# Kernel optimization log

Measured on AMD Instinct MI355X. Metric: run time of the kernel, lower is better.

## Reference

```python
import jax, jax.numpy as jnp
import numpy as np

ROPE_BASE = 10000.0


def _rope_tables(T, d, dtype):
    # inv_freq over even indices, emb = concat(freqs, freqs) -> [T, d]
    inv_freq = 1.0 / (ROPE_BASE ** (jnp.arange(0, d, 2, dtype=jnp.float32) / d))
    t = jnp.arange(T, dtype=jnp.float32)
    freqs = jnp.einsum('i,j->ij', t, inv_freq)          # [T, d/2]
    emb = jnp.concatenate([freqs, freqs], axis=-1)      # [T, d]
    return jnp.cos(emb).astype(dtype), jnp.sin(emb).astype(dtype)


def _rotate_half(x):
    d = x.shape[-1] // 2
    return jnp.concatenate([-x[..., d:], x[..., :d]], axis=-1)


def _apply_rope(x, cos, sin):
    # x: [B, T, H, Dh]; cos/sin: [T, Dh] broadcast over batch and heads
    c = cos[None, :, None, :]
    s = sin[None, :, None, :]
    return x * c + _rotate_half(x) * s


def setup_inputs() -> dict:
    key = jax.random.key(0)
    k1, k2, k3 = jax.random.split(key, 3)
    B, T, C = 2, 2048, 1024
    x = jax.random.normal(k1, (B, T, C), dtype=jnp.float32)
    # weights stored as [in, out] (transposed nn.Linear), scaled like torch init
    W_qkv = jax.random.normal(k2, (C, 3 * C), dtype=jnp.float32) * (C ** -0.5)
    W_proj = jax.random.normal(k3, (C, C), dtype=jnp.float32) * (C ** -0.5)
    return {'x': x, 'W_qkv': W_qkv, 'W_proj': W_proj}


def reference(x, W_qkv, W_proj):
    B, T, C = x.shape
    H = 16
    Dh = C // H
    qkv = x @ W_qkv                                   # [B, T, 3C]
    q, k, v = jnp.split(qkv, 3, axis=-1)
    q = q.reshape(B, T, H, Dh)
    k = k.reshape(B, T, H, Dh)
    v = v.reshape(B, T, H, Dh)
    cos, sin = _rope_tables(T, Dh, x.dtype)
    q = _apply_rope(q, cos, sin)
    k = _apply_rope(k, cos, sin)
    scale = 1.0 / jnp.sqrt(jnp.asarray(Dh, dtype=x.dtype))
    # causal SDPA: scores [B, H, T, T]
    scores = jnp.einsum('bqhd,bkhd->bhqk', q, k) * scale
    causal = jnp.tril(jnp.ones((T, T), dtype=bool))
    scores = jnp.where(causal[None, None], scores, jnp.asarray(-jnp.inf, dtype=scores.dtype))
    attn = jax.nn.softmax(scores, axis=-1)
    y = jnp.einsum('bhqk,bkhd->bqhd', attn, v).reshape(B, T, C)
    return y @ W_proj
```

## Files before the change

### kernel.cpp

```cpp
#include <hip/hip_runtime.h>
#include <cstdint>
#include <cstddef>

typedef __bf16 bf16;
typedef __bf16 bf16x2 __attribute__((ext_vector_type(2)));
typedef __bf16 bf16x4 __attribute__((ext_vector_type(4)));
typedef __bf16 bf16x8 __attribute__((ext_vector_type(8)));
typedef float  f32x4  __attribute__((ext_vector_type(4)));
typedef float  f32x16 __attribute__((ext_vector_type(16)));
typedef int    i32x4  __attribute__((ext_vector_type(4)));

__device__ __forceinline__ float fexp2(float x) {
  float r;
  asm("v_exp_f32 %0, %1" : "=v"(r) : "v"(x));
  return r;
}
__device__ __forceinline__ float m3(float a, float b, float c) {
  return fmaxf(fmaxf(a, b), c);
}

#define G2L(src, dst)                                                          \
  __builtin_amdgcn_global_load_lds(                                            \
      (const __attribute__((address_space(1))) unsigned int*)(src),            \
      (__attribute__((address_space(3))) unsigned int*)(dst), 16, 0, 0)

__global__ void k_f32_to_bf16(const float* __restrict__ in, bf16* __restrict__ out, int n) {
  int i = (blockIdx.x * blockDim.x + threadIdx.x) * 8;
  if (i >= n) return;
  float4 a = *(const float4*)(in + i);
  float4 b = *(const float4*)(in + i + 4);
  bf16x8 o;
  o[0] = (bf16)a.x; o[1] = (bf16)a.y; o[2] = (bf16)a.z; o[3] = (bf16)a.w;
  o[4] = (bf16)b.x; o[5] = (bf16)b.y; o[6] = (bf16)b.z; o[7] = (bf16)b.w;
  *(bf16x8*)(out + i) = o;
}

__global__ void k_transpose_f32_bf16(const float* __restrict__ in, bf16* __restrict__ out,
                                     int R, int C) {
  __shared__ float tile[32][33];
  int c0 = blockIdx.x * 32, r0 = blockIdx.y * 32;
  int tx = threadIdx.x & 31, ty = threadIdx.x >> 5;
#pragma unroll
  for (int i = 0; i < 32; i += 8)
    tile[ty + i][tx] = in[(size_t)(r0 + ty + i) * C + c0 + tx];
  __syncthreads();
#pragma unroll
  for (int i = 0; i < 32; i += 8)
    out[(size_t)(c0 + ty + i) * R + r0 + tx] = (bf16)tile[tx][ty + i];
}

__global__ void k_rope_tables(float* __restrict__ cosT, float* __restrict__ sinT, int total) {
  int i = blockIdx.x * blockDim.x + threadIdx.x;
  if (i >= total) return;
  int t = i >> 5, j = i & 31;
  float inv = powf(10000.0f, -(float)j * (1.0f / 32.0f));
  float f = (float)t * inv;
  cosT[i] = cosf(f);
  sinT[i] = sinf(f);
}

__global__ __launch_bounds__(256) void k_rope_v(const bf16* __restrict__ qkv,
                                                const float* __restrict__ cosT,
                                                const float* __restrict__ sinT,
                                                bf16* __restrict__ qr,
                                                bf16* __restrict__ kr,
                                                bf16* __restrict__ vt) {
  __shared__ bf16 tile[64][66];
  int bh = blockIdx.y;
  int t0 = blockIdx.x * 64;
  int b = bh >> 4, h = bh & 15;
  int tt = threadIdx.x >> 2, g = threadIdx.x & 3;
  int c4 = g * 16;
  const bf16* row = qkv + (size_t)(b * 2048 + t0 + tt) * 3072 + h * 64;
  bf16x8 v0 = *(const bf16x8*)(row + 2048 + c4);
  bf16x8 v1 = *(const bf16x8*)(row + 2048 + c4 + 8);
#pragma unroll
  for (int j = 0; j < 8; j++) { tile[tt][c4 + j] = v0[j]; tile[tt][c4 + 8 + j] = v1[j]; }
  int tglob = t0 + tt;
  size_t ob = ((size_t)bh * 2048 + tglob) * 64;
  const float QS = 0.125f * 1.44269504f;
  bf16x8 qlo = *(const bf16x8*)(row + g * 8);
  bf16x8 qhi = *(const bf16x8*)(row + 32 + g * 8);
  bf16x8 klo = *(const bf16x8*)(row + 1024 + g * 8);
  bf16x8 khi = *(const bf16x8*)(row + 1024 + 32 + g * 8);
  bf16x8 qo0, qo1, ko0, ko1;
#pragma unroll
  for (int j = 0; j < 8; j++) {
    float c = cosT[tglob * 32 + g * 8 + j], s = sinT[tglob * 32 + g * 8 + j];
    float ql = (float)qlo[j], qh = (float)qhi[j];
    float kl = (float)klo[j], kh = (float)khi[j];
    qo0[j] = (bf16)((ql * c - qh * s) * QS);
    qo1[j] = (bf16)((qh * c + ql * s) * QS);
    ko0[j] = (bf16)(kl * c - kh * s);
    ko1[j] = (bf16)(kh * c + kl * s);
  }
  *(bf16x8*)&qr[ob + g * 8]      = qo0;
  *(bf16x8*)&qr[ob + 32 + g * 8] = qo1;
  *(bf16x8*)&kr[ob + g * 8]      = ko0;
  *(bf16x8*)&kr[ob + 32 + g * 8] = ko1;
  __syncthreads();
  int d = threadIdx.x >> 2, tc0 = (threadIdx.x & 3) * 16;
  bf16x8 o0, o1;
#pragma unroll
  for (int j = 0; j < 8; j++) { o0[j] = tile[tc0 + j][d]; o1[j] = tile[tc0 + 8 + j][d]; }
  bf16* dst = vt + ((size_t)bh * 64 + d) * 2048 + t0 + tc0;
  *(bf16x8*)dst = o0;
  *(bf16x8*)(dst + 8) = o1;
}

template <int OUTF32>
__global__ __launch_bounds__(256) void k_gemm_bt(const bf16* __restrict__ A,
                                                 const bf16* __restrict__ Bt,
                                                 float* __restrict__ Cf, bf16* __restrict__ Cb,
                                                 int M, int N, int K) {
  __shared__ __align__(16) bf16 sA[128 * 64];
  __shared__ __align__(16) bf16 sB[128 * 64];
  int nwg = gridDim.x * gridDim.y;
  int idl = blockIdx.y * gridDim.x + blockIdx.x;
  int cpx = nwg >> 3;
  int swz = (idl & 7) * cpx + (idl >> 3);
  int bx = swz % gridDim.x, by = swz / gridDim.x;
  int m0 = by * 128, n0 = bx * 128;
  int t = threadIdx.x, lane = t & 63, w = t >> 6;
  int wr = w >> 1, wc = w & 1;
  int lr = lane & 15, q2 = lane >> 4;
  int srow8 = lane >> 3, pc8 = lane & 7;
  f32x4 acc[4][4] = {};
  for (int k0 = 0; k0 < K; k0 += 64) {
#pragma unroll
    for (int is = 0; is < 4; is++) {
      int r = w * 32 + is * 8 + srow8;
      int lc = pc8 ^ (r & 7);
      G2L(A + (size_t)(m0 + r) * K + k0 + lc * 8, &sA[(w * 32 + is * 8) * 64]);
    }
#pragma unroll
    for (int is = 0; is < 4; is++) {
      int r = w * 32 + is * 8 + srow8;
      int lc = pc8 ^ (r & 7);
      G2L(Bt + (size_t)(n0 + r) * K + k0 + lc * 8, &sB[(w * 32 + is * 8) * 64]);
    }
    __syncthreads();
#pragma unroll
    for (int ch = 0; ch < 2; ch++) {
      bf16x8 af[4], bfr[4];
#pragma unroll
      for (int i = 0; i < 4; i++) {
        int r = wr * 64 + i * 16 + lr;
        af[i] = *(const bf16x8*)&sA[r * 64 + (((ch * 4 + q2) ^ (r & 7)) * 8)];
      }
#pragma unroll
      for (int i = 0; i < 4; i++) {
        int r = wc * 64 + i * 16 + lr;
        bfr[i] = *(const bf16x8*)&sB[r * 64 + (((ch * 4 + q2) ^ (r & 7)) * 8)];
      }
#pragma unroll
      for (int mi = 0; mi < 4; mi++)
#pragma unroll
        for (int ni = 0; ni < 4; ni++)
          acc[mi][ni] = __builtin_amdgcn_mfma_f32_16x16x32_bf16(af[mi], bfr[ni], acc[mi][ni], 0, 0, 0);
    }
    __syncthreads();
  }
  int row_base = m0 + wr * 64, col_base = n0 + wc * 64;
#pragma unroll
  for (int mi = 0; mi < 4; mi++)
#pragma unroll
    for (int ni = 0; ni < 4; ni++) {
      int col = col_base + ni * 16 + lr;
#pragma unroll
      for (int r = 0; r < 4; r++) {
        int row = row_base + mi * 16 + q2 * 4 + r;
        float v = acc[mi][ni][r];
        if (OUTF32) Cf[(size_t)row * N + col] = v;
        else        Cb[(size_t)row * N + col] = (bf16)v;
      }
    }
}

__global__ __launch_bounds__(128) void k_flash_part(const bf16* __restrict__ qr,
                                                    const bf16* __restrict__ kr,
                                                    const bf16* __restrict__ vt,
                                                    bf16* __restrict__ Opart,
                                                    float* __restrict__ ml) {
  const int T = 2048;
  int id = blockIdx.x;
  int slot = id >> 5;
  int bh = id & 31;
  int qt = 31, c = 0;
  {
    int s = slot;
#pragma unroll 1
    for (int q = 31; q >= 0; --q) {
      int n = q / 6 + 1;
      if (s < n) { qt = q; c = s; break; }
      s -= n;
    }
  }
  int kt0 = c * 6;
  int kt1 = qt + 1 < kt0 + 6 ? qt + 1 : kt0 + 6;

  __shared__ __align__(16) bf16 sK[64 * 64];
  __shared__ __align__(16) bf16 sV[64 * 64];
  int t = threadIdx.x, lane = t & 63, w = t >> 6;
  int q31 = lane & 31, hi = lane >> 5;
  int srow8 = lane >> 3, pc8 = lane & 7;

  const bf16* Kbh = kr + (size_t)bh * T * 64;
  const bf16* Vbh = vt + (size_t)bh * 64 * T;

  int qwb = qt * 64 + w * 32;
  int qg = qwb + q31;
  const bf16* qrow = qr + ((size_t)bh * T + qg) * 64 + hi * 8;
  bf16x8 qf[4];
#pragma unroll
  for (int ks = 0; ks < 4; ks++) qf[ks] = *(const bf16x8*)(qrow + ks * 16);
  f32x16 o0 = {}, o1 = {};
  float m = -1e30f, l = 0.f;

  auto stage = [&](int kt) {
#pragma unroll
    for (int is = 0; is < 4; is++) {
      int r = w * 32 + is * 8 + srow8;
      int lc = pc8 ^ (r & 7);
      G2L(Kbh + (size_t)(kt * 64 + r) * 64 + lc * 8, &sK[(w * 32 + is * 8) * 64]);
    }
#pragma unroll
    for (int is = 0; is < 4; is++) {
      int d = w * 32 + is * 8 + srow8;
      int lc = pc8 ^ (d & 7);
      G2L(Vbh + (size_t)d * T + kt * 64 + lc * 8, &sV[(w * 32 + is * 8) * 64]);
    }
  };

  stage(kt0);
  for (int kt = kt0; kt < kt1; kt++) {
    asm volatile("s_waitcnt vmcnt(0)" ::: "memory");
    __builtin_amdgcn_s_barrier();
    asm volatile("" ::: "memory");
    __builtin_amdgcn_sched_barrier(0);
    f32x16 s[2];
    __builtin_amdgcn_s_setprio(1);
#pragma unroll
    for (int kb = 0; kb < 2; kb++) {
      f32x16 a = {};
      int krow = kb * 32 + q31;
#pragma unroll
      for (int ks = 0; ks < 4; ks++) {
        int ch = (ks * 2 + hi) ^ (krow & 7);
        bf16x8 kf = *(const bf16x8*)&sK[krow * 64 + ch * 8];
        a = __builtin_amdgcn_mfma_f32_32x32x16_bf16(kf, qf[ks], a, 0, 0, 0);
      }
      s[kb] = a;
    }
    __builtin_amdgcn_s_setprio(0);
    if (kt == qt) {
      int thr = qg - kt * 64;
#pragma unroll
      for (int kb = 0; kb < 2; kb++)
#pragma unroll
        for (int r = 0; r < 16; r++) {
          int koff = kb * 32 + (r & 3) + 8 * (r >> 2) + 4 * hi;
          if (koff > thr) s[kb][r] = -1e30f;
        }
    }
    float tm[16];
#pragma unroll
    for (int i = 0; i < 16; i++) tm[i] = fmaxf(s[0][i], s[1][i]);
    float a0 = m3(tm[0], tm[1], tm[2]);
    float a1 = m3(tm[3], tm[4], tm[5]);
    float a2 = m3(tm[6], tm[7], tm[8]);
    float a3 = m3(tm[9], tm[10], tm[11]);
    float a4 = m3(tm[12], tm[13], tm[14]);
    float b0 = m3(a0, a1, tm[15]);
    float b1 = m3(a2, a3, a4);
    float px = fmaxf(b0, b1);
    px = fmaxf(px, __shfl_xor(px, 32, 64));
    float mn = fmaxf(m, px);
    float alpha = fexp2(m - mn);
    m = mn;
    float ts[16];
#pragma unroll
    for (int i = 0; i < 16; i++) {
      float p0 = fexp2(s[0][i] - m);
      float p1 = fexp2(s[1][i] - m);
      s[0][i] = p0;
      s[1][i] = p1;
      ts[i] = p0 + p1;
    }
#pragma unroll
    for (int st = 8; st > 0; st >>= 1)
#pragma unroll
      for (int i = 0; i < st; i++) ts[i] += ts[i + st];
    float rs = ts[0];
    rs += __shfl_xor(rs, 32, 64);
    l = l * alpha + rs;
    int pw[4][4];
#pragma unroll
    for (int kb = 0; kb < 2; kb++) {
      int wd[8];
#pragma unroll
      for (int g = 0; g < 4; g++) {
        bf16x2 a, cc;
        a[0] = (bf16)s[kb][4 * g + 0]; a[1] = (bf16)s[kb][4 * g + 1];
        cc[0] = (bf16)s[kb][4 * g + 2]; cc[1] = (bf16)s[kb][4 * g + 3];
        wd[2 * g]     = __builtin_bit_cast(int, a);
        wd[2 * g + 1] = __builtin_bit_cast(int, cc);
      }
      asm volatile("v_permlane32_swap_b32 %0, %1" : "+v"(wd[0]), "+v"(wd[2]));
      asm volatile("v_permlane32_swap_b32 %0, %1" : "+v"(wd[1]), "+v"(wd[3]));
      asm volatile("v_permlane32_swap_b32 %0, %1" : "+v"(wd[4]), "+v"(wd[6]));
      asm volatile("v_permlane32_swap_b32 %0, %1" : "+v"(wd[5]), "+v"(wd[7]));
      pw[2 * kb][0] = wd[0]; pw[2 * kb][1] = wd[1];
      pw[2 * kb][2] = wd[2]; pw[2 * kb][3] = wd[3];
      pw[2 * kb + 1][0] = wd[4]; pw[2 * kb + 1][1] = wd[5];
      pw[2 * kb + 1][2] = wd[6]; pw[2 * kb + 1][3] = wd[7];
    }
#pragma unroll
    for (int r = 0; r < 16; r++) { o0[r] *= alpha; o1[r] *= alpha; }
    __builtin_amdgcn_s_setprio(1);
#pragma unroll
    for (int ks = 0; ks < 4; ks++) {
      i32x4 pv = {pw[ks][0], pw[ks][1], pw[ks][2], pw[ks][3]};
      bf16x8 pb = __builtin_bit_cast(bf16x8, pv);
      {
        int drow = q31;
        int ch = (ks * 2 + hi) ^ (drow & 7);
        bf16x8 vf = *(const bf16x8*)&sV[drow * 64 + ch * 8];
        o0 = __builtin_amdgcn_mfma_f32_32x32x16_bf16(vf, pb, o0, 0, 0, 0);
      }
      {
        int drow = 32 + q31;
        int ch = (ks * 2 + hi) ^ (drow & 7);
        bf16x8 vf = *(const bf16x8*)&sV[drow * 64 + ch * 8];
        o1 = __builtin_amdgcn_mfma_f32_32x32x16_bf16(vf, pb, o1, 0, 0, 0);
      }
    }
    __builtin_amdgcn_s_setprio(0);
    asm volatile("" ::: "memory");
    __builtin_amdgcn_s_barrier();
    asm volatile("" ::: "memory");
    if (kt + 1 < kt1) stage(kt + 1);
  }
  int qloc = w * 32 + q31;
  bf16* Ob = Opart + (size_t)id * 4096 + qloc * 64;
#pragma unroll
  for (int g = 0; g < 4; g++) {
    bf16x4 v0, v1;
#pragma unroll
    for (int j = 0; j < 4; j++) {
      v0[j] = (bf16)o0[4 * g + j];
      v1[j] = (bf16)o1[4 * g + j];
    }
    *(bf16x4*)&Ob[8 * g + 4 * hi]      = v0;
    *(bf16x4*)&Ob[32 + 8 * g + 4 * hi] = v1;
  }
  if (hi == 0) {
    ml[(size_t)id * 128 + qloc]      = m;
    ml[(size_t)id * 128 + 64 + qloc] = l;
  }
}

__global__ __launch_bounds__(256) void k_combine(const bf16* __restrict__ Opart,
                                                 const float* __restrict__ ml,
                                                 bf16* __restrict__ attn) {
  int bhqt = blockIdx.x;
  int bh = bhqt & 31, qt = bhqt >> 5;
  int b = bh >> 4, h = bh & 15;
  int nch = qt / 6 + 1;
  int slot0 = 0;
#pragma unroll 1
  for (int q = 31; q > qt; --q) slot0 += q / 6 + 1;
  int t = threadIdx.x;
  int q = t >> 2, ds = (t & 3) * 16;
  float M = -1e30f;
  for (int c = 0; c < nch; c++)
    M = fmaxf(M, ml[(size_t)((slot0 + c) * 32 + bh) * 128 + q]);
  float acc[16] = {};
  float L = 0.f;
  for (int c = 0; c < nch; c++) {
    int p = (slot0 + c) * 32 + bh;
    float wgt = fexp2(ml[(size_t)p * 128 + q] - M);
    L += wgt * ml[(size_t)p * 128 + 64 + q];
    const bf16* row = Opart + (size_t)p * 4096 + q * 64 + ds;
    bf16x8 a0 = *(const bf16x8*)row;
    bf16x8 a1 = *(const bf16x8*)(row + 8);
#pragma unroll
    for (int i = 0; i < 8; i++) {
      acc[i]     += wgt * (float)a0[i];
      acc[i + 8] += wgt * (float)a1[i];
    }
  }
  float Linv = 1.0f / L;
  bf16x8 w0, w1;
#pragma unroll
  for (int i = 0; i < 8; i++) {
    w0[i] = (bf16)(acc[i] * Linv);
    w1[i] = (bf16)(acc[i + 8] * Linv);
  }
  bf16* dst = attn + ((size_t)(b * 2048) + qt * 64 + q) * 1024 + h * 64 + ds;
  *(bf16x8*)dst = w0;
  *(bf16x8*)(dst + 8) = w1;
}

extern "C" void kernel_launch(void* const* d_in, const int* in_sizes, int n_in,
                              void* d_out, int out_size, void* d_ws, size_t ws_size,
                              hipStream_t stream) {
  const float* x     = (const float*)d_in[0];
  const float* Wqkv  = (const float*)d_in[1];
  const float* Wproj = (const float*)d_in[2];
  float* outp = (float*)d_out;
  const int B = 2, T = 2048, C = 1024;
  const int M = B * T;

  char* ws = (char*)d_ws;
  size_t off = 0;
  auto alloc = [&](size_t bytes) {
    void* p = ws + off;
    off += (bytes + 255) & ~(size_t)255;
    return p;
  };
  bf16* xb     = (bf16*)alloc((size_t)M * C * 2);
  bf16* wprojt = (bf16*)alloc((size_t)C * C * 2);
  float* cosT  = (float*)alloc((size_t)T * 32 * 4);
  float* sinT  = (float*)alloc((size_t)T * 32 * 4);
  bf16* qkv    = (bf16*)alloc((size_t)M * 3 * C * 2);
  bf16* wqkvt  = (bf16*)alloc((size_t)3 * C * C * 2);
  bf16* qr     = (bf16*)alloc((size_t)M * C * 2);
  bf16* kr     = (bf16*)alloc((size_t)M * C * 2);
  bf16* vt     = (bf16*)alloc((size_t)M * C * 2);
  bf16* attn   = xb;
  bf16* Opart  = qkv;
  float* ml    = (float*)(qkv + (size_t)3264 * 4096);

  k_f32_to_bf16<<<dim3(M * C / 8 / 256), dim3(256), 0, stream>>>(x, xb, M * C);
  k_transpose_f32_bf16<<<dim3(3 * C / 32, C / 32), dim3(256), 0, stream>>>(Wqkv, wqkvt, C, 3 * C);
  k_transpose_f32_bf16<<<dim3(C / 32, C / 32), dim3(256), 0, stream>>>(Wproj, wprojt, C, C);
  k_rope_tables<<<dim3(T * 32 / 256), dim3(256), 0, stream>>>(cosT, sinT, T * 32);
  k_gemm_bt<0><<<dim3(3 * C / 128, M / 128), dim3(256), 0, stream>>>(xb, wqkvt, (float*)nullptr, qkv, M, 3 * C, C);
  k_rope_v<<<dim3(T / 64, 32), dim3(256), 0, stream>>>(qkv, cosT, sinT, qr, kr, vt);
  k_flash_part<<<dim3(3264), dim3(128), 0, stream>>>(qr, kr, vt, Opart, ml);
  k_combine<<<dim3(1024), dim3(256), 0, stream>>>(Opart, ml, attn);
  k_gemm_bt<1><<<dim3(C / 128, M / 128), dim3(256), 0, stream>>>(attn, wprojt, outp, (bf16*)nullptr, M, C, C);
}
```

Baseline: 130.8 us.

## Prefetch next K/V tile into registers during compute instead of direct global-to-LDS loads

Replaces the direct global_load_lds staging of K and V tiles with a register prefetch issued at the start of each iteration, followed by a commit of the registers to LDS after the compute barrier. Previously the next tile's load was issued only after compute and waited on at the top of the loop. Now the global latency overlaps with the QK and PV MFMA work of the current tile. The cost is 32 extra VGPRs per thread, which may reduce occupancy, plus an extra LDS write pass and a second barrier per iteration.

```diff
diff --git a/kernel.cpp b/kernel.cpp
--- a/kernel.cpp
+++ b/kernel.cpp
@@ -217,26 +217,43 @@
   f32x16 o0 = {}, o1 = {};
   float m = -1e30f, l = 0.f;
 
-  auto stage = [&](int kt) {
+  i32x4 pk[4], pv[4];
+  auto prefetch = [&](int kt) {
 #pragma unroll
     for (int is = 0; is < 4; is++) {
       int r = w * 32 + is * 8 + srow8;
       int lc = pc8 ^ (r & 7);
-      G2L(Kbh + (size_t)(kt * 64 + r) * 64 + lc * 8, &sK[(w * 32 + is * 8) * 64]);
+      pk[is] = *(const i32x4*)(Kbh + (size_t)(kt * 64 + r) * 64 + lc * 8);
     }
 #pragma unroll
     for (int is = 0; is < 4; is++) {
       int d = w * 32 + is * 8 + srow8;
       int lc = pc8 ^ (d & 7);
-      G2L(Vbh + (size_t)d * T + kt * 64 + lc * 8, &sV[(w * 32 + is * 8) * 64]);
+      pv[is] = *(const i32x4*)(Vbh + (size_t)d * T + kt * 64 + lc * 8);
     }
   };
-
-  stage(kt0);
+  auto commit = [&]() {
+#pragma unroll
+    for (int is = 0; is < 4; is++) {
+      int r = w * 32 + is * 8 + srow8;
+      *(i32x4*)&sK[r * 64 + pc8 * 8] = pk[is];
+    }
+#pragma unroll
+    for (int is = 0; is < 4; is++) {
+      int d = w * 32 + is * 8 + srow8;
+      *(i32x4*)&sV[d * 64 + pc8 * 8] = pv[is];
+    }
+  };
+
+  prefetch(kt0);
+  commit();
+  asm volatile("s_waitcnt lgkmcnt(0)" ::: "memory");
+  __builtin_amdgcn_s_barrier();
+  asm volatile("" ::: "memory");
+
   for (int kt = kt0; kt < kt1; kt++) {
-    asm volatile("s_waitcnt vmcnt(0)" ::: "memory");
-    __builtin_amdgcn_s_barrier();
-    asm volatile("" ::: "memory");
+    bool more = (kt + 1 < kt1);
+    if (more) prefetch(kt + 1);
     __builtin_amdgcn_sched_barrier(0);
     f32x16 s[2];
     __builtin_amdgcn_s_setprio(1);
@@ -320,8 +337,8 @@
     __builtin_amdgcn_s_setprio(1);
 #pragma unroll
     for (int ks = 0; ks < 4; ks++) {
-      i32x4 pv = {pw[ks][0], pw[ks][1], pw[ks][2], pw[ks][3]};
-      bf16x8 pb = __builtin_bit_cast(bf16x8, pv);
+      i32x4 pvv = {pw[ks][0], pw[ks][1], pw[ks][2], pw[ks][3]};
+      bf16x8 pb = __builtin_bit_cast(bf16x8, pvv);
       {
         int drow = q31;
         int ch = (ks * 2 + hi) ^ (drow & 7);
@@ -339,7 +356,12 @@
     asm volatile("" ::: "memory");
     __builtin_amdgcn_s_barrier();
     asm volatile("" ::: "memory");
-    if (kt + 1 < kt1) stage(kt + 1);
+    if (more) {
+      commit();
+      asm volatile("s_waitcnt lgkmcnt(0)" ::: "memory");
+      __builtin_amdgcn_s_barrier();
+      asm volatile("" ::: "memory");
+    }
   }
   int qloc = w * 32 + q31;
   bf16* Ob = Opart + (size_t)id * 4096 + qloc * 64;
```

Result: slower. 134.8 us (+3.1%).
